# Kernel tuning notes

Hardware: AMD Instinct MI355X
Metric: run time of the kernel (lower is better)

The kernel has to match this reference:

```python
import jax, jax.numpy as jnp
import numpy as np

BS, N, H = 16, 128, 256
L, F = 9, 48  # lat_embed_dim, frac_embed_dim = 6*frac_freq
IN_DIM = 2 * H + L + F


def setup_inputs() -> dict:
    key = jax.random.key(0)
    ks = jax.random.split(key, 7)
    node_embed = jax.random.normal(ks[0], (BS, N, H), dtype=jnp.float32)
    edge_embed = jax.random.normal(ks[1], (BS, N, N, F), dtype=jnp.float32)
    graph_embed = jax.random.normal(ks[2], (BS, L), dtype=jnp.float32)
    s1 = 1.0 / np.sqrt(IN_DIM)
    s2 = 1.0 / np.sqrt(H)
    W1 = jax.random.uniform(ks[3], (IN_DIM, H), jnp.float32, -s1, s1)
    b1 = jax.random.uniform(ks[4], (H,), jnp.float32, -s1, s1)
    W2 = jax.random.uniform(ks[5], (H, H), jnp.float32, -s2, s2)
    b2 = jax.random.uniform(ks[6], (H,), jnp.float32, -s2, s2)
    return {"node_embed": node_embed, "edge_embed": edge_embed,
            "graph_embed": graph_embed, "W1": W1, "b1": b1, "W2": W2, "b2": b2}


def reference(node_embed, edge_embed, graph_embed, W1, b1, W2, b2):
    bs, n, h = node_embed.shape
    # Concat order matches torch: [node_j, node_i, graph, edge_ij]
    # First linear is applied to the concat; split W1 by segment so we never
    # materialize the (bs, N, N, 2H+L+F) concat tensor (same math).
    Wj = W1[:h]            # acts on node_embed[b, j]
    Wi = W1[h:2 * h]       # acts on node_embed[b, i]
    Wg = W1[2 * h:2 * h + L]  # acts on graph_embed[b]
    We = W1[2 * h + L:]    # acts on edge_embed[b, i, j]
    pj = node_embed @ Wj                      # (bs, N, H) -> broadcast over i
    pi = node_embed @ Wi                      # (bs, N, H) -> broadcast over j
    pg = graph_embed @ Wg                     # (bs, H)
    pe = jnp.einsum('bijf,fh->bijh', edge_embed, We)  # (bs, N, N, H)
    z1 = pe + pj[:, None, :, :] + pi[:, :, None, :] + pg[:, None, None, :] + b1
    h1 = jax.nn.silu(z1)
    edge_msg = jax.nn.silu(h1 @ W2 + b2)      # (bs, N, N, H)
    node_msg = edge_msg.mean(axis=2)          # mean over j
    return node_msg
```

## Files before the change

### kernel.cpp

```cpp
#include <hip/hip_runtime.h>

#define BSZ 16
#define NN  128
#define HH  256
#define LLG 9
#define FFE 48

typedef float        f32x4 __attribute__((ext_vector_type(4)));
typedef _Float16     f16x8 __attribute__((ext_vector_type(8)));
typedef unsigned int u32x4 __attribute__((ext_vector_type(4)));

static __device__ __forceinline__ unsigned short f2h_bits(float x) {
    _Float16 h = (_Float16)x;
    return __builtin_bit_cast(unsigned short, h);
}

static __device__ __forceinline__ float fast_silu(float x) {
    float e = __builtin_amdgcn_exp2f(x * -1.44269504088896341f);
    return x * __builtin_amdgcn_rcpf(1.0f + e);
}

__global__ __launch_bounds__(256) void pre_w(
    const float* __restrict__ W1, const float* __restrict__ W2,
    unsigned short* __restrict__ W2T, unsigned short* __restrict__ WeT)
{
    int tid = blockIdx.x * 256 + threadIdx.x;
    {
        int ho = tid >> 8, k = tid & 255;
        W2T[(ho << 8) + k] = f2h_bits(W2[(k << 8) + ho]);
    }
    if (tid < 256 * 64) {
        int h = tid >> 6, f = tid & 63;
        WeT[(h << 6) + f] = (f < FFE) ? f2h_bits(W1[(521 + f) * HH + h])
                                      : (unsigned short)0;
    }
}

__global__ __launch_bounds__(256) void pre_pjbase(
    const float* __restrict__ node, const float* __restrict__ graph,
    const float* __restrict__ W1, const float* __restrict__ b1,
    float* __restrict__ pj, float* __restrict__ base)
{
    __shared__ float nrow[4][HH];
    __shared__ float gsh[LLG];
    const int blk = blockIdx.x;
    const int b = blk >> 5;
    const int r0 = (blk & 31) << 2;
    const int h = threadIdx.x;

    for (int t = h; t < 4 * HH; t += 256) {
        int r = t >> 8, k = t & 255;
        nrow[r][k] = node[(((size_t)b * NN) + r0 + r) * HH + k];
    }
    if (h < LLG) gsh[h] = graph[b * LLG + h];
    __syncthreads();

    float accj[4] = {0,0,0,0};
    float acci[4] = {0,0,0,0};
    for (int k = 0; k < HH; ++k) {
        float wj = W1[k * HH + h];
        float wi = W1[(k + HH) * HH + h];
        #pragma unroll
        for (int r = 0; r < 4; ++r) {
            float nv = nrow[r][k];
            accj[r] = fmaf(nv, wj, accj[r]);
            acci[r] = fmaf(nv, wi, acci[r]);
        }
    }
    float accg = b1[h];
    #pragma unroll
    for (int l = 0; l < LLG; ++l)
        accg = fmaf(gsh[l], W1[(2 * HH + l) * HH + h], accg);

    #pragma unroll
    for (int r = 0; r < 4; ++r) {
        size_t off = (((size_t)b * NN) + r0 + r) * HH + h;
        pj[off]   = accj[r];
        base[off] = acci[r] + accg;
    }
}

__global__ __launch_bounds__(512, 4) void fused_msg(
    const float* __restrict__ edge, const float* __restrict__ pj,
    const float* __restrict__ base, const unsigned short* __restrict__ W2T,
    const unsigned short* __restrict__ WeT, const float* __restrict__ b2,
    float* __restrict__ out)
{
    __shared__ unsigned char h1s[NN * HH * 2];
    __shared__ unsigned char efs[NN * 64 * 2];
    const int tid  = threadIdx.x;
    const int w    = tid >> 6;
    const int lane = tid & 63;
    const int q    = lane >> 4;
    const int c    = lane & 15;
    const int g    = blockIdx.x;
    const int bi   = ((g & 7) << 8) + (g >> 3);
    const int b    = bi >> 7;

    const float* eb = edge + (size_t)bi * (NN * FFE);

    #pragma unroll
    for (int p = 0; p < 3; ++p) {
        const int e4 = p * 512 + tid;
        const int j  = e4 / 12;
        const int f4 = e4 - j * 12;
        const f32x4 x = *reinterpret_cast<const f32x4*>(eb + (e4 << 2));
        unsigned int lo = __builtin_bit_cast(unsigned int,
                            __builtin_amdgcn_cvt_pkrtz(x[0], x[1]));
        unsigned int hi = __builtin_bit_cast(unsigned int,
                            __builtin_amdgcn_cvt_pkrtz(x[2], x[3]));
        const unsigned int off = (unsigned)(j << 7) +
            (((unsigned)(f4 << 3)) ^ ((unsigned)(j & 7) << 4));
        *reinterpret_cast<uint2*>(&efs[off]) = make_uint2(lo, hi);
    }
    {
        const int j = tid >> 2, gg = tid & 3;
        const unsigned int off = (unsigned)(j << 7) +
            (((unsigned)(96 + (gg << 3))) ^ ((unsigned)(j & 7) << 4));
        *reinterpret_cast<uint2*>(&efs[off]) = make_uint2(0u, 0u);
    }
    __syncthreads();

    f32x4 acc1[2][8];
    #pragma unroll
    for (int mt = 0; mt < 2; ++mt)
        #pragma unroll
        for (int nt = 0; nt < 8; ++nt) acc1[mt][nt] = f32x4{0.f, 0.f, 0.f, 0.f};

    #pragma unroll
    for (int kk = 0; kk < 2; ++kk) {
        const int koff = (kk << 5) + (q << 3);
        const int fb   = koff << 1;
        f16x8 af[2];
        #pragma unroll
        for (int mt = 0; mt < 2; ++mt) {
            const int row = (w << 5) + (mt << 4) + c;
            af[mt] = *reinterpret_cast<const f16x8*>(WeT + (row << 6) + koff);
        }
        #pragma unroll
        for (int nt = 0; nt < 8; ++nt) {
            const int j = (nt << 4) + c;
            const f16x8 bf = *reinterpret_cast<const f16x8*>(
                &efs[(unsigned)(j << 7) +
                     (((unsigned)fb) ^ ((unsigned)(j & 7) << 4))]);
            #pragma unroll
            for (int mt = 0; mt < 2; ++mt)
                acc1[mt][nt] = __builtin_amdgcn_mfma_f32_16x16x32_f16(
                    af[mt], bf, acc1[mt][nt], 0, 0, 0);
        }
    }

    #pragma unroll
    for (int mt = 0; mt < 2; ++mt) {
        const int h0 = (w << 5) + (mt << 4) + (q << 2);
        const f32x4 bb = *reinterpret_cast<const f32x4*>(
            base + ((size_t)bi << 8) + h0);
        #pragma unroll
        for (int nt = 0; nt < 8; ++nt) {
            const int jc = (nt << 4) + c;
            const f32x4 pjv = *reinterpret_cast<const f32x4*>(
                pj + (((size_t)b << 7) + jc) * HH + h0);
            float s0 = fast_silu(acc1[mt][nt][0] + bb[0] + pjv[0]);
            float s1 = fast_silu(acc1[mt][nt][1] + bb[1] + pjv[1]);
            float s2 = fast_silu(acc1[mt][nt][2] + bb[2] + pjv[2]);
            float s3 = fast_silu(acc1[mt][nt][3] + bb[3] + pjv[3]);
            unsigned int lo = __builtin_bit_cast(unsigned int,
                                __builtin_amdgcn_cvt_pkrtz(s0, s1));
            unsigned int hi = __builtin_bit_cast(unsigned int,
                                __builtin_amdgcn_cvt_pkrtz(s2, s3));
            const unsigned int off = (unsigned)(jc << 9) +
                (((unsigned)(h0 << 1)) ^ ((unsigned)(jc & 7) << 4));
            *reinterpret_cast<uint2*>(&h1s[off]) = make_uint2(lo, hi);
        }
    }
    __syncthreads();

    f32x4 acc2[8][2];
    #pragma unroll
    for (int mt = 0; mt < 8; ++mt)
        #pragma unroll
        for (int nt = 0; nt < 2; ++nt) acc2[mt][nt] = f32x4{0.f, 0.f, 0.f, 0.f};

    #pragma unroll 2
    for (int kk = 0; kk < 8; ++kk) {
        const int kb = (kk << 6) + (q << 4);
        f16x8 bw[2];
        #pragma unroll
        for (int nt = 0; nt < 2; ++nt) {
            const int ho = (w << 5) + (nt << 4) + c;
            bw[nt] = *reinterpret_cast<const f16x8*>(
                W2T + (ho << 8) + (kk << 5) + (q << 3));
        }
        #pragma unroll
        for (int gg = 0; gg < 2; ++gg) {
            f16x8 a2[4];
            #pragma unroll
            for (int m = 0; m < 4; ++m) {
                const int jc = ((gg << 2) + m) * 16 + c;
                const unsigned int off = (unsigned)(jc << 9) +
                    (((unsigned)kb) ^ ((unsigned)(jc & 7) << 4));
                a2[m] = *reinterpret_cast<const f16x8*>(&h1s[off]);
            }
            #pragma unroll
            for (int m = 0; m < 4; ++m)
                #pragma unroll
                for (int nt = 0; nt < 2; ++nt)
                    acc2[(gg << 2) + m][nt] = __builtin_amdgcn_mfma_f32_16x16x32_f16(
                        a2[m], bw[nt], acc2[(gg << 2) + m][nt], 0, 0, 0);
        }
    }

    float b2v[2];
    #pragma unroll
    for (int nt = 0; nt < 2; ++nt) b2v[nt] = b2[(w << 5) + (nt << 4) + c];

    float s[2] = {0.f, 0.f};
    #pragma unroll
    for (int nt = 0; nt < 2; ++nt)
        #pragma unroll
        for (int mt = 0; mt < 8; ++mt)
            #pragma unroll
            for (int r = 0; r < 4; ++r)
                s[nt] += fast_silu(acc2[mt][nt][r] + b2v[nt]);

    #pragma unroll
    for (int nt = 0; nt < 2; ++nt) {
        s[nt] += __shfl_xor(s[nt], 16);
        s[nt] += __shfl_xor(s[nt], 32);
    }
    if (q < 2)
        out[((size_t)bi << 8) + (w << 5) + (q << 4) + c] = s[q] * 0.0078125f;
}

extern "C" void kernel_launch(void* const* d_in, const int* in_sizes, int n_in,
                              void* d_out, int out_size, void* d_ws, size_t ws_size,
                              hipStream_t stream)
{
    const float* node  = (const float*)d_in[0];
    const float* edge  = (const float*)d_in[1];
    const float* graph = (const float*)d_in[2];
    const float* W1    = (const float*)d_in[3];
    const float* b1    = (const float*)d_in[4];
    const float* W2    = (const float*)d_in[5];
    const float* b2    = (const float*)d_in[6];
    float* out = (float*)d_out;

    char* ws = (char*)d_ws;
    unsigned short* W2T = (unsigned short*)ws;
    unsigned short* WeT = (unsigned short*)(ws + 131072);
    float* pj   = (float*)(ws + 163840);
    float* base = (float*)(ws + 163840 + 2097152);

    pre_w     <<<256, 256, 0, stream>>>(W1, W2, W2T, WeT);
    pre_pjbase<<<512, 256, 0, stream>>>(node, graph, W1, b1, pj, base);
    fused_msg <<<BSZ * NN, 512, 0, stream>>>(edge, pj, base, W2T, WeT, b2, out);
}
```

Measured before the change: 107.3 us.

## Split fused message kernel over halves of j with partial-sum combine pass

The fused per-(b,i) kernel is split into two blocks per row, each handling 64 of the 128 j neighbours with 256 threads and half the LDS (64KB+8KB instead of 128KB+16KB). Each warp now covers 64 output channels with 4x4 MFMA tiles, and partial sums are written to a workspace, then added and scaled by a separate combine kernel. The aim is more resident blocks per CU and better occupancy and latency hiding. The cost is an extra launch, an extra global round trip for the partials, and W2/We fragment loads duplicated across twice as many blocks.

```diff
diff --git a/kernel.cpp b/kernel.cpp
--- a/kernel.cpp
+++ b/kernel.cpp
@@ -80,28 +80,30 @@
     }
 }
 
-__global__ __launch_bounds__(512, 4) void fused_msg(
+__global__ __launch_bounds__(256, 4) void fused_half(
     const float* __restrict__ edge, const float* __restrict__ pj,
     const float* __restrict__ base, const unsigned short* __restrict__ W2T,
     const unsigned short* __restrict__ WeT, const float* __restrict__ b2,
-    float* __restrict__ out)
-{
-    __shared__ unsigned char h1s[NN * HH * 2];
-    __shared__ unsigned char efs[NN * 64 * 2];
+    float* __restrict__ part)
+{
+    __shared__ unsigned char h1s[64 * HH * 2];
+    __shared__ unsigned char efs[64 * 64 * 2];
     const int tid  = threadIdx.x;
     const int w    = tid >> 6;
     const int lane = tid & 63;
     const int q    = lane >> 4;
     const int c    = lane & 15;
     const int g    = blockIdx.x;
-    const int bi   = ((g & 7) << 8) + (g >> 3);
+    const int gid  = ((g & 7) << 9) + (g >> 3);
+    const int bi   = gid >> 1;
+    const int half = gid & 1;
     const int b    = bi >> 7;
 
-    const float* eb = edge + (size_t)bi * (NN * FFE);
+    const float* eb = edge + (size_t)bi * (NN * FFE) + half * (64 * FFE);
 
     #pragma unroll
     for (int p = 0; p < 3; ++p) {
-        const int e4 = p * 512 + tid;
+        const int e4 = p * 256 + tid;
         const int j  = e4 / 12;
         const int f4 = e4 - j * 12;
         const f32x4 x = *reinterpret_cast<const f32x4*>(eb + (e4 << 2));
@@ -121,45 +123,46 @@
     }
     __syncthreads();
 
-    f32x4 acc1[2][8];
-    #pragma unroll
-    for (int mt = 0; mt < 2; ++mt)
-        #pragma unroll
-        for (int nt = 0; nt < 8; ++nt) acc1[mt][nt] = f32x4{0.f, 0.f, 0.f, 0.f};
+    f32x4 acc1[4][4];
+    #pragma unroll
+    for (int mt = 0; mt < 4; ++mt)
+        #pragma unroll
+        for (int nt = 0; nt < 4; ++nt) acc1[mt][nt] = f32x4{0.f, 0.f, 0.f, 0.f};
 
     #pragma unroll
     for (int kk = 0; kk < 2; ++kk) {
         const int koff = (kk << 5) + (q << 3);
         const int fb   = koff << 1;
-        f16x8 af[2];
-        #pragma unroll
-        for (int mt = 0; mt < 2; ++mt) {
-            const int row = (w << 5) + (mt << 4) + c;
+        f16x8 af[4];
+        #pragma unroll
+        for (int mt = 0; mt < 4; ++mt) {
+            const int row = (w << 6) + (mt << 4) + c;
             af[mt] = *reinterpret_cast<const f16x8*>(WeT + (row << 6) + koff);
         }
         #pragma unroll
-        for (int nt = 0; nt < 8; ++nt) {
+        for (int nt = 0; nt < 4; ++nt) {
             const int j = (nt << 4) + c;
             const f16x8 bf = *reinterpret_cast<const f16x8*>(
                 &efs[(unsigned)(j << 7) +
                      (((unsigned)fb) ^ ((unsigned)(j & 7) << 4))]);
             #pragma unroll
-            for (int mt = 0; mt < 2; ++mt)
+            for (int mt = 0; mt < 4; ++mt)
                 acc1[mt][nt] = __builtin_amdgcn_mfma_f32_16x16x32_f16(
                     af[mt], bf, acc1[mt][nt], 0, 0, 0);
         }
     }
 
     #pragma unroll
-    for (int mt = 0; mt < 2; ++mt) {
-        const int h0 = (w << 5) + (mt << 4) + (q << 2);
+    for (int mt = 0; mt < 4; ++mt) {
+        const int h0 = (w << 6) + (mt << 4) + (q << 2);
         const f32x4 bb = *reinterpret_cast<const f32x4*>(
             base + ((size_t)bi << 8) + h0);
         #pragma unroll
-        for (int nt = 0; nt < 8; ++nt) {
+        for (int nt = 0; nt < 4; ++nt) {
             const int jc = (nt << 4) + c;
+            const int jg = (half << 6) + jc;
             const f32x4 pjv = *reinterpret_cast<const f32x4*>(
-                pj + (((size_t)b << 7) + jc) * HH + h0);
+                pj + (((size_t)b << 7) + jg) * HH + h0);
             float s0 = fast_silu(acc1[mt][nt][0] + bb[0] + pjv[0]);
             float s1 = fast_silu(acc1[mt][nt][1] + bb[1] + pjv[1]);
             float s2 = fast_silu(acc1[mt][nt][2] + bb[2] + pjv[2]);
@@ -175,61 +178,62 @@
     }
     __syncthreads();
 
-    f32x4 acc2[8][2];
-    #pragma unroll
-    for (int mt = 0; mt < 8; ++mt)
-        #pragma unroll
-        for (int nt = 0; nt < 2; ++nt) acc2[mt][nt] = f32x4{0.f, 0.f, 0.f, 0.f};
+    f32x4 acc2[4][4];
+    #pragma unroll
+    for (int m = 0; m < 4; ++m)
+        #pragma unroll
+        for (int nt = 0; nt < 4; ++nt) acc2[m][nt] = f32x4{0.f, 0.f, 0.f, 0.f};
 
     #pragma unroll 2
     for (int kk = 0; kk < 8; ++kk) {
         const int kb = (kk << 6) + (q << 4);
-        f16x8 bw[2];
-        #pragma unroll
-        for (int nt = 0; nt < 2; ++nt) {
-            const int ho = (w << 5) + (nt << 4) + c;
+        f16x8 bw[4];
+        #pragma unroll
+        for (int nt = 0; nt < 4; ++nt) {
+            const int ho = (w << 6) + (nt << 4) + c;
             bw[nt] = *reinterpret_cast<const f16x8*>(
                 W2T + (ho << 8) + (kk << 5) + (q << 3));
         }
-        #pragma unroll
-        for (int gg = 0; gg < 2; ++gg) {
-            f16x8 a2[4];
+        f16x8 a2[4];
+        #pragma unroll
+        for (int m = 0; m < 4; ++m) {
+            const int jc = (m << 4) + c;
+            const unsigned int off = (unsigned)(jc << 9) +
+                (((unsigned)kb) ^ ((unsigned)(jc & 7) << 4));
+            a2[m] = *reinterpret_cast<const f16x8*>(&h1s[off]);
+        }
+        #pragma unroll
+        for (int m = 0; m < 4; ++m)
             #pragma unroll
-            for (int m = 0; m < 4; ++m) {
-                const int jc = ((gg << 2) + m) * 16 + c;
-                const unsigned int off = (unsigned)(jc << 9) +
-                    (((unsigned)kb) ^ ((unsigned)(jc & 7) << 4));
-                a2[m] = *reinterpret_cast<const f16x8*>(&h1s[off]);
-            }
-            #pragma unroll
-            for (int m = 0; m < 4; ++m)
-                #pragma unroll
-                for (int nt = 0; nt < 2; ++nt)
-                    acc2[(gg << 2) + m][nt] = __builtin_amdgcn_mfma_f32_16x16x32_f16(
-                        a2[m], bw[nt], acc2[(gg << 2) + m][nt], 0, 0, 0);
-        }
-    }
-
-    float b2v[2];
-    #pragma unroll
-    for (int nt = 0; nt < 2; ++nt) b2v[nt] = b2[(w << 5) + (nt << 4) + c];
-
-    float s[2] = {0.f, 0.f};
-    #pragma unroll
-    for (int nt = 0; nt < 2; ++nt)
-        #pragma unroll
-        for (int mt = 0; mt < 8; ++mt)
+            for (int nt = 0; nt < 4; ++nt)
+                acc2[m][nt] = __builtin_amdgcn_mfma_f32_16x16x32_f16(
+                    a2[m], bw[nt], acc2[m][nt], 0, 0, 0);
+    }
+
+    float s[4] = {0.f, 0.f, 0.f, 0.f};
+    #pragma unroll
+    for (int nt = 0; nt < 4; ++nt) {
+        const float b2v = b2[(w << 6) + (nt << 4) + c];
+        #pragma unroll
+        for (int m = 0; m < 4; ++m)
             #pragma unroll
             for (int r = 0; r < 4; ++r)
-                s[nt] += fast_silu(acc2[mt][nt][r] + b2v[nt]);
-
-    #pragma unroll
-    for (int nt = 0; nt < 2; ++nt) {
+                s[nt] += fast_silu(acc2[m][nt][r] + b2v);
+    }
+    #pragma unroll
+    for (int nt = 0; nt < 4; ++nt) {
         s[nt] += __shfl_xor(s[nt], 16);
         s[nt] += __shfl_xor(s[nt], 32);
     }
-    if (q < 2)
-        out[((size_t)bi << 8) + (w << 5) + (q << 4) + c] = s[q] * 0.0078125f;
+    const float v = (q == 0) ? s[0] : (q == 1) ? s[1] : (q == 2) ? s[2] : s[3];
+    part[((size_t)half << 19) + ((size_t)bi << 8) + (w << 6) + lane] = v;
+}
+
+__global__ __launch_bounds__(256) void combine(
+    const float* __restrict__ part, float* __restrict__ out)
+{
+    const int i = blockIdx.x * 256 + threadIdx.x;
+    out[i] = (part[i] + part[(1 << 19) + i]) * 0.0078125f;
 }
 
 extern "C" void kernel_launch(void* const* d_in, const int* in_sizes, int n_in,
@@ -250,8 +254,10 @@
     unsigned short* WeT = (unsigned short*)(ws + 131072);
     float* pj   = (float*)(ws + 163840);
     float* base = (float*)(ws + 163840 + 2097152);
+    float* part = (float*)(ws + 163840 + 2097152 + 2097152);
 
     pre_w     <<<256, 256, 0, stream>>>(W1, W2, W2T, WeT);
     pre_pjbase<<<512, 256, 0, stream>>>(node, graph, W1, b1, pj, base);
-    fused_msg <<<BSZ * NN, 512, 0, stream>>>(edge, pj, base, W2T, WeT, b2, out);
-}
+    fused_half<<<2 * BSZ * NN, 256, 0, stream>>>(edge, pj, base, W2T, WeT, b2, part);
+    combine   <<<2048, 256, 0, stream>>>(part, out);
+}
```

Measured after the change: 140.5 us. 30.9% more time.

## Compute node projections with fp16 MFMA and precompute graph term

Applied to the files above, without the earlier changes.

Replaces the scalar fp32 FMA loop computing pj and base with an MFMA-based fp16 GEMM. The kernel uses a transposed fp16 copy of the node-related W1 slices and stages node rows in swizzled LDS. The graph/bias term pg is now computed once per batch in the preprocessing kernel instead of in every block. This aims to cut the time of the pre-pass, which previously did roughly 2*2048*256*256 scalar FMAs, in exchange for fp16 rounding of node_embed and W1, and 64 blocks that may underfill the GPU.

```diff
diff --git a/kernel.cpp b/kernel.cpp
--- a/kernel.cpp
+++ b/kernel.cpp
@@ -22,61 +22,119 @@
 
 __global__ __launch_bounds__(256) void pre_w(
     const float* __restrict__ W1, const float* __restrict__ W2,
-    unsigned short* __restrict__ W2T, unsigned short* __restrict__ WeT)
+    const float* __restrict__ graph, const float* __restrict__ b1,
+    unsigned short* __restrict__ W2T, unsigned short* __restrict__ WeT,
+    unsigned short* __restrict__ W1jiT, float* __restrict__ pg)
 {
-    int tid = blockIdx.x * 256 + threadIdx.x;
-    {
+    const int blk = blockIdx.x;
+    const int t   = threadIdx.x;
+    if (blk < 256) {
+        int tid = blk * 256 + t;
         int ho = tid >> 8, k = tid & 255;
         W2T[(ho << 8) + k] = f2h_bits(W2[(k << 8) + ho]);
-    }
-    if (tid < 256 * 64) {
-        int h = tid >> 6, f = tid & 63;
-        WeT[(h << 6) + f] = (f < FFE) ? f2h_bits(W1[(521 + f) * HH + h])
-                                      : (unsigned short)0;
-    }
-}
-
-__global__ __launch_bounds__(256) void pre_pjbase(
-    const float* __restrict__ node, const float* __restrict__ graph,
-    const float* __restrict__ W1, const float* __restrict__ b1,
+        if (tid < 256 * 64) {
+            int h = tid >> 6, f = tid & 63;
+            WeT[(h << 6) + f] = (f < FFE) ? f2h_bits(W1[(521 + f) * HH + h])
+                                          : (unsigned short)0;
+        }
+    } else if (blk < 768) {
+        int tid = (blk - 256) * 256 + t;
+        int hp = tid >> 8, f = tid & 255;
+        int src = (((hp >> 8) << 8) + f) * HH + (hp & 255);
+        W1jiT[(hp << 8) + f] = f2h_bits(W1[src]);
+    } else {
+        int b = blk - 768;
+        float acc = b1[t];
+        #pragma unroll
+        for (int l = 0; l < LLG; ++l)
+            acc = fmaf(graph[b * LLG + l], W1[(2 * HH + l) * HH + t], acc);
+        pg[(b << 8) + t] = acc;
+    }
+}
+
+__global__ __launch_bounds__(256) void pre_pjbase_mfma(
+    const float* __restrict__ node, const unsigned short* __restrict__ W1jiT,
+    const float* __restrict__ pg,
     float* __restrict__ pj, float* __restrict__ base)
 {
-    __shared__ float nrow[4][HH];
-    __shared__ float gsh[LLG];
-    const int blk = blockIdx.x;
-    const int b = blk >> 5;
-    const int r0 = (blk & 31) << 2;
-    const int h = threadIdx.x;
-
-    for (int t = h; t < 4 * HH; t += 256) {
-        int r = t >> 8, k = t & 255;
-        nrow[r][k] = node[(((size_t)b * NN) + r0 + r) * HH + k];
-    }
-    if (h < LLG) gsh[h] = graph[b * LLG + h];
+    __shared__ unsigned char nls[32 * 512];
+    const int tid = threadIdx.x;
+    const int w    = tid >> 6;
+    const int lane = tid & 63;
+    const int q    = lane >> 4;
+    const int c    = lane & 15;
+    const int b  = blockIdx.x >> 2;
+    const int r0 = (blockIdx.x & 3) << 5;
+    const unsigned ck = (unsigned)(c & 7) << 4;
+
+    const float* nb = node + (((size_t)b << 7) + r0) * HH;
+    #pragma unroll
+    for (int p = 0; p < 8; ++p) {
+        const int e4 = (p << 8) + tid;
+        const int r  = e4 >> 6, f4 = e4 & 63;
+        const f32x4 x = *reinterpret_cast<const f32x4*>(nb + (e4 << 2));
+        unsigned int lo = __builtin_bit_cast(unsigned int,
+                            __builtin_amdgcn_cvt_pkrtz(x[0], x[1]));
+        unsigned int hi = __builtin_bit_cast(unsigned int,
+                            __builtin_amdgcn_cvt_pkrtz(x[2], x[3]));
+        const unsigned off = (unsigned)(r << 9) +
+            (((unsigned)(f4 << 3)) ^ ((unsigned)(r & 7) << 4));
+        *reinterpret_cast<uint2*>(&nls[off]) = make_uint2(lo, hi);
+    }
     __syncthreads();
 
-    float accj[4] = {0,0,0,0};
-    float acci[4] = {0,0,0,0};
-    for (int k = 0; k < HH; ++k) {
-        float wj = W1[k * HH + h];
-        float wi = W1[(k + HH) * HH + h];
-        #pragma unroll
-        for (int r = 0; r < 4; ++r) {
-            float nv = nrow[r][k];
-            accj[r] = fmaf(nv, wj, accj[r]);
-            acci[r] = fmaf(nv, wi, acci[r]);
-        }
-    }
-    float accg = b1[h];
-    #pragma unroll
-    for (int l = 0; l < LLG; ++l)
-        accg = fmaf(gsh[l], W1[(2 * HH + l) * HH + h], accg);
-
-    #pragma unroll
-    for (int r = 0; r < 4; ++r) {
-        size_t off = (((size_t)b * NN) + r0 + r) * HH + h;
-        pj[off]   = accj[r];
-        base[off] = acci[r] + accg;
+    const int wh = w << 7;
+    f32x4 acc[8][2];
+    #pragma unroll
+    for (int mt = 0; mt < 8; ++mt)
+        #pragma unroll
+        for (int nt = 0; nt < 2; ++nt) acc[mt][nt] = f32x4{0.f, 0.f, 0.f, 0.f};
+
+    #pragma unroll 2
+    for (int kk = 0; kk < 8; ++kk) {
+        const unsigned kb = (unsigned)((kk << 6) + (q << 4));
+        f16x8 bfr[2];
+        #pragma unroll
+        for (int nt = 0; nt < 2; ++nt) {
+            const int r = (nt << 4) + c;
+            bfr[nt] = *reinterpret_cast<const f16x8*>(
+                &nls[(unsigned)(r << 9) + (kb ^ ck)]);
+        }
+        #pragma unroll
+        for (int mt = 0; mt < 8; ++mt) {
+            const f16x8 af = *reinterpret_cast<const f16x8*>(
+                W1jiT + ((wh + (mt << 4) + c) << 8) + (kk << 5) + (q << 3));
+            #pragma unroll
+            for (int nt = 0; nt < 2; ++nt)
+                acc[mt][nt] = __builtin_amdgcn_mfma_f32_16x16x32_f16(
+                    af, bfr[nt], acc[mt][nt], 0, 0, 0);
+        }
+    }
+
+    if (w < 2) {
+        #pragma unroll
+        for (int mt = 0; mt < 8; ++mt) {
+            const int hb = wh + (mt << 4) + (q << 2);
+            #pragma unroll
+            for (int nt = 0; nt < 2; ++nt) {
+                const int r = r0 + (nt << 4) + c;
+                *reinterpret_cast<f32x4*>(
+                    pj + (((size_t)b << 7) + r) * HH + hb) = acc[mt][nt];
+            }
+        }
+    } else {
+        #pragma unroll
+        for (int mt = 0; mt < 8; ++mt) {
+            const int hb = wh - 256 + (mt << 4) + (q << 2);
+            const f32x4 pgv = *reinterpret_cast<const f32x4*>(
+                pg + (b << 8) + hb);
+            #pragma unroll
+            for (int nt = 0; nt < 2; ++nt) {
+                const int r = r0 + (nt << 4) + c;
+                *reinterpret_cast<f32x4*>(
+                    base + (((size_t)b << 7) + r) * HH + hb) = acc[mt][nt] + pgv;
+            }
+        }
     }
 }
 
@@ -246,12 +304,14 @@
     float* out = (float*)d_out;
 
     char* ws = (char*)d_ws;
-    unsigned short* W2T = (unsigned short*)ws;
-    unsigned short* WeT = (unsigned short*)(ws + 131072);
-    float* pj   = (float*)(ws + 163840);
-    float* base = (float*)(ws + 163840 + 2097152);
-
-    pre_w     <<<256, 256, 0, stream>>>(W1, W2, W2T, WeT);
-    pre_pjbase<<<512, 256, 0, stream>>>(node, graph, W1, b1, pj, base);
-    fused_msg <<<BSZ * NN, 512, 0, stream>>>(edge, pj, base, W2T, WeT, b2, out);
-}
+    unsigned short* W2T   = (unsigned short*)ws;
+    unsigned short* WeT   = (unsigned short*)(ws + 131072);
+    unsigned short* W1jiT = (unsigned short*)(ws + 163840);
+    float* pg   = (float*)(ws + 425984);
+    float* pj   = (float*)(ws + 442368);
+    float* base = (float*)(ws + 442368 + 2097152);
+
+    pre_w          <<<784, 256, 0, stream>>>(W1, W2, graph, b1, W2T, WeT, W1jiT, pg);
+    pre_pjbase_mfma<<< 64, 256, 0, stream>>>(node, W1jiT, pg, pj, base);
+    fused_msg      <<<BSZ * NN, 512, 0, stream>>>(edge, pj, base, W2T, WeT, b2, out);
+}
```

Result: faster. 100.1 us (median of 2 runs) (-6.8%).
